# Performance work log

Hardware: AMD Instinct MI355X
Metric: run time of the kernel (lower is better)

Reference implementation:

```python
import jax, jax.numpy as jnp
import numpy as np

D_MODEL = 512
N_HEADS = 4
D_HEAD = D_MODEL // N_HEADS
D_FF = 2048
N_LAYERS = 3
IN_DIM = 25
OUT_DIM = 1
PRE = 20          # pre_training_size
SCALE = 10.0      # scaling_factor
EPS = 1e-5


def setup_inputs() -> dict:
    key = jax.random.key(0)
    ks = jax.random.split(key, 20)
    B, S = 4, 2048
    def gn(k, shape, fan_in):
        return jax.random.normal(k, shape, jnp.float32) * (1.0 / np.sqrt(fan_in))
    return {
        "src": jax.random.normal(ks[0], (B, S, IN_DIM), jnp.float32),
        "emb_w": gn(ks[1], (D_MODEL, IN_DIM), IN_DIM),
        "emb_b": jnp.zeros((D_MODEL,), jnp.float32),
        "in_w": gn(ks[2], (N_LAYERS, 3 * D_MODEL, D_MODEL), D_MODEL),
        "in_b": jnp.zeros((N_LAYERS, 3 * D_MODEL), jnp.float32),
        "out_w": gn(ks[3], (N_LAYERS, D_MODEL, D_MODEL), D_MODEL),
        "out_b": jnp.zeros((N_LAYERS, D_MODEL), jnp.float32),
        "ln1_g": jnp.ones((N_LAYERS, D_MODEL), jnp.float32),
        "ln1_b": jnp.zeros((N_LAYERS, D_MODEL), jnp.float32),
        "ln2_g": jnp.ones((N_LAYERS, D_MODEL), jnp.float32),
        "ln2_b": jnp.zeros((N_LAYERS, D_MODEL), jnp.float32),
        "ff1_w": gn(ks[4], (N_LAYERS, D_FF, D_MODEL), D_MODEL),
        "ff1_b": jnp.zeros((N_LAYERS, D_FF), jnp.float32),
        "ff2_w": gn(ks[5], (N_LAYERS, D_MODEL, D_FF), D_FF),
        "ff2_b": jnp.zeros((N_LAYERS, D_MODEL), jnp.float32),
        "dec_w": gn(ks[6], (OUT_DIM, D_MODEL), D_MODEL),
        "dec_b": jnp.zeros((OUT_DIM,), jnp.float32),
    }


def _layer_norm(x, g, b):
    mu = jnp.mean(x, axis=-1, keepdims=True)
    var = jnp.var(x, axis=-1, keepdims=True)
    return (x - mu) * jax.lax.rsqrt(var + EPS) * g + b


def _pos_encoding(seq_len):
    # eval mode: start index 0, no dropout
    pos = jnp.arange(seq_len, dtype=jnp.float32)[:, None]           # [S,1]
    div = jnp.exp(jnp.arange(0, D_MODEL, 2, dtype=jnp.float32) * (-np.log(10000.0) / D_MODEL))  # [D/2]
    ang = pos * div                                                  # [S,D/2]
    return jnp.stack([jnp.sin(ang), jnp.cos(ang)], axis=-1).reshape(seq_len, D_MODEL)


def _causal_mask(seq_len):
    row = jnp.arange(seq_len)[:, None]
    col = jnp.arange(seq_len)[None, :]
    mask = jnp.where(col <= row, 0.0, -jnp.inf).astype(jnp.float32)
    # include_training_period=True: first PRE x PRE block unmasked
    return mask.at[:PRE, :PRE].set(0.0)


def reference(src, emb_w, emb_b, in_w, in_b, out_w, out_b,
              ln1_g, ln1_b, ln2_g, ln2_b, ff1_w, ff1_b, ff2_w, ff2_b,
              dec_w, dec_b):
    B, S, _ = src.shape
    x = src @ emb_w.T + emb_b                    # [B,S,D]
    x = x + _pos_encoding(S)[None]
    mask = _causal_mask(S)                       # [S,S]
    scale = 1.0 / np.sqrt(D_HEAD)
    for l in range(N_LAYERS):
        # --- self-attention (post-norm, eager bmm+softmax+bmm path) ---
        qkv = x @ in_w[l].T + in_b[l]            # [B,S,3D]
        q, k, v = jnp.split(qkv, 3, axis=-1)
        q = q.reshape(B, S, N_HEADS, D_HEAD).transpose(0, 2, 1, 3)
        k = k.reshape(B, S, N_HEADS, D_HEAD).transpose(0, 2, 1, 3)
        v = v.reshape(B, S, N_HEADS, D_HEAD).transpose(0, 2, 1, 3)
        scores = jnp.einsum('bhqd,bhkd->bhqk', q, k) * scale + mask
        attn = jax.nn.softmax(scores, axis=-1)   # [B,H,S,S] (need_weights=True path)
        o = jnp.einsum('bhqk,bhkd->bhqd', attn, v)
        o = o.transpose(0, 2, 1, 3).reshape(B, S, D_MODEL)
        o = o @ out_w[l].T + out_b[l]
        x = _layer_norm(x + o, ln1_g[l], ln1_b[l])
        # --- FFN ---
        h = jax.nn.relu(x @ ff1_w[l].T + ff1_b[l])
        h = h @ ff2_w[l].T + ff2_b[l]
        x = _layer_norm(x + h, ln2_g[l], ln2_b[l])
    out = jnp.tanh(x @ dec_w.T + dec_b) * SCALE  # [B,S,1]
    return out
```

## Files before the change

kernel.cpp:

```cpp
#include <hip/hip_runtime.h>

#define S_LEN 2048
#define DMODEL 512

typedef __attribute__((ext_vector_type(8))) short bf16x8;
typedef __attribute__((ext_vector_type(4))) float f32x4;
typedef __attribute__((ext_vector_type(4))) unsigned short u16x4;
typedef __attribute__((ext_vector_type(8))) unsigned short u16x8;
typedef __attribute__((ext_vector_type(2))) unsigned int u32x2;

__device__ __forceinline__ unsigned short f2bf(float f) {
    unsigned int u = __float_as_uint(f);
    u += 0x7fff + ((u >> 16) & 1);
    return (unsigned short)(u >> 16);
}
__device__ __forceinline__ float bf2f(unsigned short h) {
    return __uint_as_float(((unsigned int)h) << 16);
}
__device__ __forceinline__ void gll16(const void* g, void* l) {
    __builtin_amdgcn_global_load_lds(
        (const __attribute__((address_space(1))) unsigned int*)g,
        (__attribute__((address_space(3))) unsigned int*)l, 16, 0, 0);
}

__global__ __launch_bounds__(256) void conv_bf16(const float4* __restrict__ in,
                                                 u16x4* __restrict__ out)
{
    int i = blockIdx.x * 256 + threadIdx.x;
    float4 v = in[i];
    u16x4 o = { f2bf(v.x), f2bf(v.y), f2bf(v.z), f2bf(v.w) };
    out[i] = o;
}

__global__ __launch_bounds__(256) void embed_kernel(
    const float* __restrict__ src, const float* __restrict__ ew,
    const float* __restrict__ eb, float* __restrict__ X,
    unsigned short* __restrict__ Xb)
{
    int rid = blockIdx.x;
    int s = rid & (S_LEN - 1);
    int tid = threadIdx.x;
    __shared__ float sr[25];
    if (tid < 25) sr[tid] = src[rid * 25 + tid];
    __syncthreads();
    #pragma unroll
    for (int rep = 0; rep < 2; rep++) {
        int d = tid + rep * 256;
        float a = eb[d];
        #pragma unroll
        for (int k = 0; k < 25; k++) a = fmaf(sr[k], ew[d * 25 + k], a);
        int i2 = d & ~1;
        float div = expf(-(float)i2 * (9.210340371976184f / 512.f));
        float ang = (float)s * div;
        a += (d & 1) ? cosf(ang) : sinf(ang);
        X[(size_t)rid * DMODEL + d] = a;
        Xb[(size_t)rid * DMODEL + d] = f2bf(a);
    }
}

template<int MODE, int BN>
__global__ __launch_bounds__(256) void gemm_bf16(
    const unsigned short* __restrict__ A, int lda,
    const unsigned short* __restrict__ W, int K,
    const float* __restrict__ bias,
    unsigned short* __restrict__ out, int ldc,
    unsigned short* __restrict__ out2)
{
    constexpr int NJ = BN / 32;
    __shared__ __align__(16) unsigned short As[128 * 64];
    __shared__ __align__(16) unsigned short Ws[BN * 64];
    int tid = threadIdx.x;
    int lane = tid & 63, w = tid >> 6;
    int g = lane >> 4, c15 = lane & 15;
    int wm = w >> 1, wn = w & 1;
    int bm, bn;
    if (BN == 64) {
        int raw = blockIdx.x;
        int lid = ((raw & 7) << 6) | (raw >> 3);
        bn = lid & 7; bm = lid >> 3;
    } else {
        bm = blockIdx.y; bn = blockIdx.x;
    }

    f32x4 acc[4][NJ];
    #pragma unroll
    for (int i = 0; i < 4; i++)
        #pragma unroll
        for (int j = 0; j < NJ; j++) acc[i][j] = (f32x4){0.f, 0.f, 0.f, 0.f};

    const int nk = K >> 6;
    for (int kk = 0; kk < nk; kk++) {
        __syncthreads();
        #pragma unroll
        for (int i = 0; i < 4; i++) {
            int chunk = tid + i * 256;
            int r = chunk >> 3, c = chunk & 7;
            int cs = c ^ (r & 7);
            gll16(A + (size_t)(bm * 128 + r) * lda + kk * 64 + cs * 8,
                  (void*)(As + chunk * 8));
        }
        #pragma unroll
        for (int i = 0; i < BN / 32; i++) {
            int chunk = tid + i * 256;
            int r = chunk >> 3, c = chunk & 7;
            int cs = c ^ (r & 7);
            gll16(W + (size_t)(bn * BN + r) * K + kk * 64 + cs * 8,
                  (void*)(Ws + chunk * 8));
        }
        __syncthreads();
        bf16x8 a[4][2], b[NJ][2];
        #pragma unroll
        for (int mi = 0; mi < 4; mi++) {
            int row = wm * 64 + mi * 16 + c15;
            #pragma unroll
            for (int h = 0; h < 2; h++) {
                int ck = (h * 4 + g) ^ (row & 7);
                a[mi][h] = *(const bf16x8*)((const char*)As + row * 128 + ck * 16);
            }
        }
        #pragma unroll
        for (int nj = 0; nj < NJ; nj++) {
            int row = wn * (BN / 2) + nj * 16 + c15;
            #pragma unroll
            for (int h = 0; h < 2; h++) {
                int ck = (h * 4 + g) ^ (row & 7);
                b[nj][h] = *(const bf16x8*)((const char*)Ws + row * 128 + ck * 16);
            }
        }
        __builtin_amdgcn_s_setprio(1);
        #pragma unroll
        for (int h = 0; h < 2; h++)
            #pragma unroll
            for (int mi = 0; mi < 4; mi++)
                #pragma unroll
                for (int nj = 0; nj < NJ; nj++)
                    acc[mi][nj] = __builtin_amdgcn_mfma_f32_16x16x32_bf16(
                        a[mi][h], b[nj][h], acc[mi][nj], 0, 0, 0);
        __builtin_amdgcn_s_setprio(0);
    }
    #pragma unroll
    for (int nj = 0; nj < NJ; nj++) {
        int colb = bn * BN + wn * (BN / 2) + nj * 16;
        float bv = bias[colb + c15];
        #pragma unroll
        for (int mi = 0; mi < 4; mi++) {
            int rowb = bm * 128 + wm * 64 + mi * 16 + g * 4;
            if (MODE == 3 && colb >= 1024) {
                int cv = colb - 1024 + c15;
                int hh = cv >> 7, d = cv & 127;
                int bb = rowb >> 11, t = rowb & (S_LEN - 1);
                u16x4 pk;
                #pragma unroll
                for (int r = 0; r < 4; r++) pk[r] = f2bf(acc[mi][nj][r] + bv);
                *(u16x4*)(out2 + ((size_t)(bb * 4 + hh) * 128 + d) * S_LEN + t) = pk;
            } else {
                #pragma unroll
                for (int r = 0; r < 4; r++) {
                    float v = acc[mi][nj][r] + bv;
                    if (MODE == 2) v = fmaxf(v, 0.f);
                    out[(size_t)(rowb + r) * ldc + colb + c15] = f2bf(v);
                }
            }
        }
    }
}

__global__ __launch_bounds__(256) void flash_attn(
    const unsigned short* __restrict__ QKb,
    const unsigned short* __restrict__ Vt,
    unsigned short* __restrict__ Ob,
    unsigned short* __restrict__ Opart,
    float* __restrict__ Mpart,
    float* __restrict__ Lpart)
{
    __shared__ __align__(16) unsigned short Ks[2][64 * 128];
    __shared__ __align__(16) unsigned short Vts[2][128 * 64];
    __shared__ __align__(16) unsigned short Plds[4][16 * 72];
    const float scale = 0.08838834764831845f;
    int tid = threadIdx.x;
    int lane = tid & 63, w = tid >> 6;
    int g = lane >> 4, c15 = lane & 15;
    int raw = blockIdx.x;
    int lid = (raw & 7) * 96 + (raw >> 3);
    int bh = lid / 48, idx = lid - bh * 48;
    int b = bh >> 2, h = bh & 3;
    int qb, kt0, nkt, split;
    if (idx < 16) { qb = idx; kt0 = 0; nkt = qb + 1; split = -1; }
    else {
        int s = idx - 16;
        qb = 16 + (s >> 1);
        int j = s & 1;
        int n = qb + 1, c0 = (n + 1) >> 1;
        kt0 = j ? c0 : 0;
        nkt = j ? (n - c0) : c0;
        split = bh * 32 + (qb - 16) * 2 + j;
    }

    bf16x8 q[4];
    {
        const unsigned short* qrow =
            QKb + (size_t)(b * S_LEN + qb * 64 + w * 16 + c15) * 1024 + h * 128;
        #pragma unroll
        for (int k0 = 0; k0 < 4; k0++) q[k0] = *(const bf16x8*)(qrow + k0 * 32 + g * 8);
    }
    f32x4 o[8];
    #pragma unroll
    for (int cd = 0; cd < 8; cd++) o[cd] = (f32x4){0.f, 0.f, 0.f, 0.f};
    float m = -3e38f, l = 0.f;

    auto stage = [&](int kt, int bi) {
        #pragma unroll
        for (int i = 0; i < 4; i++) {
            int chunk = tid + i * 256;
            int r = chunk >> 4, c = chunk & 15;
            int cs = (c & 8) | ((c ^ r) & 7);
            gll16(QKb + (size_t)(b * S_LEN + kt * 64 + r) * 1024 + 512 + h * 128 + cs * 8,
                  (void*)(Ks[bi] + chunk * 8));
        }
        #pragma unroll
        for (int i = 0; i < 4; i++) {
            int chunk = tid + i * 256;
            int r = chunk >> 3, c = chunk & 7;
            int cs = (c ^ r) & 7;
            gll16(Vt + ((size_t)(b * 4 + h) * 128 + r) * S_LEN + kt * 64 + cs * 8,
                  (void*)(Vts[bi] + chunk * 8));
        }
    };

    stage(kt0, 0);
    __syncthreads();
    int buf = 0;

    for (int t = 0; t < nkt; t++) {
        int kt = kt0 + t;
        if (t + 1 < nkt) stage(kt + 1, buf ^ 1);
        f32x4 sf[4];
        __builtin_amdgcn_s_setprio(1);
        #pragma unroll
        for (int c = 0; c < 4; c++) {
            sf[c] = (f32x4){0.f, 0.f, 0.f, 0.f};
            int tok16 = c * 16 + c15;
            #pragma unroll
            for (int k0 = 0; k0 < 4; k0++) {
                int ck = k0 * 4 + g;
                int cs = (ck & 8) | ((ck ^ tok16) & 7);
                bf16x8 kf = *(const bf16x8*)((const char*)Ks[buf] + tok16 * 256 + cs * 16);
                sf[c] = __builtin_amdgcn_mfma_f32_16x16x32_bf16(kf, q[k0], sf[c], 0, 0, 0);
            }
        }
        __builtin_amdgcn_s_setprio(0);
        if (kt == qb) {
            int qr = qb * 64 + w * 16 + c15;
            #pragma unroll
            for (int c = 0; c < 4; c++)
                #pragma unroll
                for (int r = 0; r < 4; r++) {
                    int tok = kt * 64 + c * 16 + g * 4 + r;
                    bool ok = (tok <= qr) || (qr < 20 && tok < 20);
                    if (!ok) sf[c][r] = -3e38f;
                }
        }
        float t0 = fmaxf(fmaxf(sf[0][0], sf[0][1]), fmaxf(sf[0][2], sf[0][3]));
        float t1 = fmaxf(fmaxf(sf[1][0], sf[1][1]), fmaxf(sf[1][2], sf[1][3]));
        float t2 = fmaxf(fmaxf(sf[2][0], sf[2][1]), fmaxf(sf[2][2], sf[2][3]));
        float t3 = fmaxf(fmaxf(sf[3][0], sf[3][1]), fmaxf(sf[3][2], sf[3][3]));
        float mt = fmaxf(fmaxf(t0, t1), fmaxf(t2, t3));
        mt = fmaxf(mt, __shfl_xor(mt, 16));
        mt = fmaxf(mt, __shfl_xor(mt, 32));
        bool need = !__all(mt <= m + 90.5f);
        float sc = 1.f;
        if (need) {
            float mn = fmaxf(m, mt);
            sc = __expf((m - mn) * scale);
            m = mn;
        }
        float msc = m * scale;
        #pragma unroll
        for (int c = 0; c < 4; c++)
            #pragma unroll
            for (int r = 0; r < 4; r++)
                sf[c][r] = __expf(fmaf(sf[c][r], scale, -msc));
        float s0 = (sf[0][0] + sf[0][1]) + (sf[0][2] + sf[0][3]);
        float s1 = (sf[1][0] + sf[1][1]) + (sf[1][2] + sf[1][3]);
        float s2 = (sf[2][0] + sf[2][1]) + (sf[2][2] + sf[2][3]);
        float s3 = (sf[3][0] + sf[3][1]) + (sf[3][2] + sf[3][3]);
        float ls = (s0 + s1) + (s2 + s3);
        ls += __shfl_xor(ls, 16);
        ls += __shfl_xor(ls, 32);
        if (need) l *= sc;
        l += ls;
        #pragma unroll
        for (int c = 0; c < 4; c++) {
            unsigned int lo = ((unsigned int)f2bf(sf[c][1]) << 16) | f2bf(sf[c][0]);
            unsigned int hi = ((unsigned int)f2bf(sf[c][3]) << 16) | f2bf(sf[c][2]);
            u32x2 pk = {lo, hi};
            *(u32x2*)&Plds[w][c15 * 72 + c * 16 + g * 4] = pk;
        }
        if (need) {
            float r0 = __shfl(sc, g * 4 + 0);
            float r1 = __shfl(sc, g * 4 + 1);
            float r2 = __shfl(sc, g * 4 + 2);
            float r3 = __shfl(sc, g * 4 + 3);
            #pragma unroll
            for (int cd = 0; cd < 8; cd++) {
                o[cd][0] *= r0; o[cd][1] *= r1; o[cd][2] *= r2; o[cd][3] *= r3;
            }
        }
        bf16x8 pa0 = *(const bf16x8*)((const char*)&Plds[w][0] + c15 * 144 + g * 16);
        bf16x8 pa1 = *(const bf16x8*)((const char*)&Plds[w][0] + c15 * 144 + 64 + g * 16);
        __builtin_amdgcn_s_setprio(1);
        #pragma unroll
        for (int cd = 0; cd < 8; cd++) {
            int dv = cd * 16 + c15;
            int csa = (g ^ dv) & 7;
            bf16x8 vfa = *(const bf16x8*)((const char*)Vts[buf] + dv * 128 + csa * 16);
            o[cd] = __builtin_amdgcn_mfma_f32_16x16x32_bf16(pa0, vfa, o[cd], 0, 0, 0);
            int csb = ((4 + g) ^ dv) & 7;
            bf16x8 vfb = *(const bf16x8*)((const char*)Vts[buf] + dv * 128 + csb * 16);
            o[cd] = __builtin_amdgcn_mfma_f32_16x16x32_bf16(pa1, vfb, o[cd], 0, 0, 0);
        }
        __builtin_amdgcn_s_setprio(0);
        __syncthreads();
        buf ^= 1;
    }

    if (split < 0) {
        float li0 = 1.f / __shfl(l, g * 4 + 0);
        float li1 = 1.f / __shfl(l, g * 4 + 1);
        float li2 = 1.f / __shfl(l, g * 4 + 2);
        float li3 = 1.f / __shfl(l, g * 4 + 3);
        size_t obase = (size_t)(b * S_LEN + qb * 64 + w * 16 + g * 4) * 512 + h * 128;
        #pragma unroll
        for (int cd = 0; cd < 8; cd++) {
            Ob[obase + 0 * 512 + cd * 16 + c15] = f2bf(o[cd][0] * li0);
            Ob[obase + 1 * 512 + cd * 16 + c15] = f2bf(o[cd][1] * li1);
            Ob[obase + 2 * 512 + cd * 16 + c15] = f2bf(o[cd][2] * li2);
            Ob[obase + 3 * 512 + cd * 16 + c15] = f2bf(o[cd][3] * li3);
        }
    } else {
        unsigned short* op = Opart + (size_t)split * 8192;
        int rb = w * 16 + g * 4;
        #pragma unroll
        for (int cd = 0; cd < 8; cd++) {
            op[(rb + 0) * 128 + cd * 16 + c15] = f2bf(o[cd][0]);
            op[(rb + 1) * 128 + cd * 16 + c15] = f2bf(o[cd][1]);
            op[(rb + 2) * 128 + cd * 16 + c15] = f2bf(o[cd][2]);
            op[(rb + 3) * 128 + cd * 16 + c15] = f2bf(o[cd][3]);
        }
        if (g == 0) {
            Mpart[split * 64 + w * 16 + c15] = m;
            Lpart[split * 64 + w * 16 + c15] = l;
        }
    }
}

__global__ __launch_bounds__(256) void attn_merge(
    const unsigned short* __restrict__ Opart,
    const float* __restrict__ Mpart, const float* __restrict__ Lpart,
    unsigned short* __restrict__ Ob)
{
    const float scale = 0.08838834764831845f;
    int bid = blockIdx.x;
    int bh = bid >> 4, qe = bid & 15;
    int qb = 16 + qe;
    int b = bh >> 2, h = bh & 3;
    int p0 = bh * 32 + qe * 2;
    int t = threadIdx.x;
    int r = t >> 2, dq = t & 3;
    float m0 = Mpart[p0 * 64 + r], m1 = Mpart[(p0 + 1) * 64 + r];
    float l0 = Lpart[p0 * 64 + r], l1 = Lpart[(p0 + 1) * 64 + r];
    float ms = fmaxf(m0, m1);
    float w0 = __expf((m0 - ms) * scale), w1 = __expf((m1 - ms) * scale);
    float linv = 1.f / (l0 * w0 + l1 * w1);
    w0 *= linv; w1 *= linv;
    const unsigned short* o0 = Opart + (size_t)p0 * 8192 + r * 128 + dq * 32;
    const unsigned short* o1 = o0 + 8192;
    unsigned short* od = Ob + (size_t)(b * S_LEN + qb * 64 + r) * 512 + h * 128 + dq * 32;
    #pragma unroll
    for (int i = 0; i < 4; i++) {
        u16x8 a = *(const u16x8*)(o0 + i * 8);
        u16x8 c = *(const u16x8*)(o1 + i * 8);
        u16x8 d;
        #pragma unroll
        for (int j = 0; j < 8; j++)
            d[j] = f2bf(bf2f(a[j]) * w0 + bf2f(c[j]) * w1);
        *(u16x8*)(od + i * 8) = d;
    }
}

__global__ __launch_bounds__(256) void add_ln_kernel(
    float* __restrict__ X, const unsigned short* __restrict__ D,
    const float* __restrict__ gw, const float* __restrict__ bw,
    unsigned short* __restrict__ Xb)
{
    int row = blockIdx.x;
    int tid = threadIdx.x;
    size_t base = (size_t)row * DMODEL;
    float v0 = X[base + tid] + bf2f(D[base + tid]);
    float v1 = X[base + tid + 256] + bf2f(D[base + tid + 256]);
    float s = v0 + v1;
    float sq = v0 * v0 + v1 * v1;
    #pragma unroll
    for (int off = 32; off > 0; off >>= 1) {
        s  += __shfl_down(s, off);
        sq += __shfl_down(sq, off);
    }
    __shared__ float red[2][4];
    int wv = tid >> 6;
    if ((tid & 63) == 0) { red[0][wv] = s; red[1][wv] = sq; }
    __syncthreads();
    s  = red[0][0] + red[0][1] + red[0][2] + red[0][3];
    sq = red[1][0] + red[1][1] + red[1][2] + red[1][3];
    float mu = s * (1.f / DMODEL);
    float var = sq * (1.f / DMODEL) - mu * mu;
    float rs = rsqrtf(var + 1e-5f);
    float y0 = (v0 - mu) * rs * gw[tid] + bw[tid];
    float y1 = (v1 - mu) * rs * gw[tid + 256] + bw[tid + 256];
    X[base + tid] = y0;
    X[base + tid + 256] = y1;
    Xb[base + tid] = f2bf(y0);
    Xb[base + tid + 256] = f2bf(y1);
}

__global__ __launch_bounds__(256) void decoder_kernel(
    const float* __restrict__ X, const float* __restrict__ w,
    const float* __restrict__ bias, float* __restrict__ out)
{
    int tid = threadIdx.x;
    int lane = tid & 63;
    int row = blockIdx.x * 4 + (tid >> 6);
    float s = 0.f;
    size_t base = (size_t)row * DMODEL;
    #pragma unroll
    for (int i = 0; i < 8; i++) s = fmaf(X[base + lane + i * 64], w[lane + i * 64], s);
    #pragma unroll
    for (int off = 32; off > 0; off >>= 1) s += __shfl_down(s, off);
    if (lane == 0) out[row] = tanhf(s + bias[0]) * 10.0f;
}

extern "C" void kernel_launch(void* const* d_in, const int* in_sizes, int n_in,
                              void* d_out, int out_size, void* d_ws, size_t ws_size,
                              hipStream_t stream)
{
    const float* src   = (const float*)d_in[0];
    const float* emb_w = (const float*)d_in[1];
    const float* emb_b = (const float*)d_in[2];
    const float* in_w  = (const float*)d_in[3];
    const float* in_b  = (const float*)d_in[4];
    const float* out_w = (const float*)d_in[5];
    const float* out_b = (const float*)d_in[6];
    const float* ln1_g = (const float*)d_in[7];
    const float* ln1_b = (const float*)d_in[8];
    const float* ln2_g = (const float*)d_in[9];
    const float* ln2_b = (const float*)d_in[10];
    const float* ff1_w = (const float*)d_in[11];
    const float* ff1_b = (const float*)d_in[12];
    const float* ff2_w = (const float*)d_in[13];
    const float* ff2_b = (const float*)d_in[14];
    const float* dec_w = (const float*)d_in[15];
    const float* dec_b = (const float*)d_in[16];

    char* ws = (char*)d_ws;
    float*          X   = (float*)ws;
    unsigned short* Xb  = (unsigned short*)(ws + (16u << 20));
    unsigned short* Pb  = (unsigned short*)(ws + (24u << 20));
    unsigned short* Ob  = (unsigned short*)(ws + (32u << 20));
    unsigned short* QKb = (unsigned short*)(ws + (40u << 20));
    unsigned short* Vt  = (unsigned short*)(ws + (56u << 20));
    unsigned short* Hb  = (unsigned short*)(ws + (40u << 20));
    unsigned short* Opart = (unsigned short*)(ws + (16u << 20));
    float* Mpart = (float*)(ws + (24u << 20));
    float* Lpart = Mpart + 512 * 64;
    unsigned short* in_wb  = (unsigned short*)(ws + (72u << 20));
    unsigned short* out_wb = in_wb  + 3u * 1536 * 512;
    unsigned short* ff1_wb = out_wb + 3u * 512 * 512;
    unsigned short* ff2_wb = ff1_wb + 3u * 2048 * 512;
    float* outp = (float*)d_out;
    const int M = 4 * S_LEN;

    conv_bf16<<<2304, 256, 0, stream>>>((const float4*)in_w,  (u16x4*)in_wb);
    conv_bf16<<<768,  256, 0, stream>>>((const float4*)out_w, (u16x4*)out_wb);
    conv_bf16<<<3072, 256, 0, stream>>>((const float4*)ff1_w, (u16x4*)ff1_wb);
    conv_bf16<<<3072, 256, 0, stream>>>((const float4*)ff2_w, (u16x4*)ff2_wb);

    embed_kernel<<<M, 256, 0, stream>>>(src, emb_w, emb_b, X, Xb);

    for (int l = 0; l < 3; l++) {
        gemm_bf16<3, 128><<<dim3(12, 64), 256, 0, stream>>>(
            Xb, 512, in_wb + (size_t)l * 1536 * 512, 512, in_b + l * 1536,
            QKb, 1024, Vt);
        flash_attn<<<768, 256, 0, stream>>>(QKb, Vt, Ob, Opart, Mpart, Lpart);
        attn_merge<<<256, 256, 0, stream>>>(Opart, Mpart, Lpart, Ob);
        gemm_bf16<1, 64><<<dim3(512), 256, 0, stream>>>(
            Ob, 512, out_wb + (size_t)l * 512 * 512, 512, out_b + l * 512,
            Pb, 512, nullptr);
        add_ln_kernel<<<M, 256, 0, stream>>>(X, Pb, ln1_g + l * 512, ln1_b + l * 512, Xb);
        gemm_bf16<2, 128><<<dim3(16, 64), 256, 0, stream>>>(
            Xb, 512, ff1_wb + (size_t)l * 2048 * 512, 512, ff1_b + l * 2048,
            Hb, 2048, nullptr);
        gemm_bf16<1, 64><<<dim3(512), 256, 0, stream>>>(
            Hb, 2048, ff2_wb + (size_t)l * 512 * 2048, 2048, ff2_b + l * 512,
            Pb, 512, nullptr);
        add_ln_kernel<<<M, 256, 0, stream>>>(X, Pb, ln2_g + l * 512, ln2_b + l * 512, Xb);
    }

    decoder_kernel<<<M / 4, 256, 0, stream>>>(X, dec_w, dec_b, outp);
}
```

Baseline: 571.5 us.

## Load K/V fragments directly from global in flash attention; merge weight conversions

Flash attention no longer stages K and V tiles into double-buffered LDS through global_load_lds. Each wave now reads its MFMA operand fragments straight from global memory (relying on cache) and drops the per-tile block barrier. This removes the LDS footprint and the synchronisation, which can raise occupancy. The cost is redundant global and cache traffic, since all four waves read the same K/V, plus exposed load latency with no prefetch. Separately, the four weight conversion launches are fused into one kernel to cut launch overhead.

```diff
diff --git a/kernel.cpp b/kernel.cpp
--- a/kernel.cpp
+++ b/kernel.cpp
@@ -23,13 +23,21 @@
         (__attribute__((address_space(3))) unsigned int*)l, 16, 0, 0);
 }
 
-__global__ __launch_bounds__(256) void conv_bf16(const float4* __restrict__ in,
-                                                 u16x4* __restrict__ out)
+__global__ __launch_bounds__(256) void conv_all(
+    const float4* __restrict__ in_w, const float4* __restrict__ out_w,
+    const float4* __restrict__ ff1_w, const float4* __restrict__ ff2_w,
+    u16x4* __restrict__ in_wb, u16x4* __restrict__ out_wb,
+    u16x4* __restrict__ ff1_wb, u16x4* __restrict__ ff2_wb)
 {
     int i = blockIdx.x * 256 + threadIdx.x;
-    float4 v = in[i];
+    const float4* src; u16x4* dst; int j;
+    if (i < 589824)        { src = in_w;  dst = in_wb;  j = i; }
+    else if (i < 786432)   { src = out_w; dst = out_wb; j = i - 589824; }
+    else if (i < 1572864)  { src = ff1_w; dst = ff1_wb; j = i - 786432; }
+    else                   { src = ff2_w; dst = ff2_wb; j = i - 1572864; }
+    float4 v = src[j];
     u16x4 o = { f2bf(v.x), f2bf(v.y), f2bf(v.z), f2bf(v.w) };
-    out[i] = o;
+    dst[j] = o;
 }
 
 __global__ __launch_bounds__(256) void embed_kernel(
@@ -173,8 +181,6 @@
     float* __restrict__ Mpart,
     float* __restrict__ Lpart)
 {
-    __shared__ __align__(16) unsigned short Ks[2][64 * 128];
-    __shared__ __align__(16) unsigned short Vts[2][128 * 64];
     __shared__ __align__(16) unsigned short Plds[4][16 * 72];
     const float scale = 0.08838834764831845f;
     int tid = threadIdx.x;
@@ -196,6 +202,9 @@
         split = bh * 32 + (qb - 16) * 2 + j;
     }
 
+    const unsigned short* Kbase = QKb + (size_t)b * S_LEN * 1024 + 512 + h * 128;
+    const unsigned short* Vbase = Vt + (size_t)(b * 4 + h) * 128 * S_LEN;
+
     bf16x8 q[4];
     {
         const unsigned short* qrow =
@@ -208,43 +217,17 @@
     for (int cd = 0; cd < 8; cd++) o[cd] = (f32x4){0.f, 0.f, 0.f, 0.f};
     float m = -3e38f, l = 0.f;
 
-    auto stage = [&](int kt, int bi) {
-        #pragma unroll
-        for (int i = 0; i < 4; i++) {
-            int chunk = tid + i * 256;
-            int r = chunk >> 4, c = chunk & 15;
-            int cs = (c & 8) | ((c ^ r) & 7);
-            gll16(QKb + (size_t)(b * S_LEN + kt * 64 + r) * 1024 + 512 + h * 128 + cs * 8,
-                  (void*)(Ks[bi] + chunk * 8));
-        }
-        #pragma unroll
-        for (int i = 0; i < 4; i++) {
-            int chunk = tid + i * 256;
-            int r = chunk >> 3, c = chunk & 7;
-            int cs = (c ^ r) & 7;
-            gll16(Vt + ((size_t)(b * 4 + h) * 128 + r) * S_LEN + kt * 64 + cs * 8,
-                  (void*)(Vts[bi] + chunk * 8));
-        }
-    };
-
-    stage(kt0, 0);
-    __syncthreads();
-    int buf = 0;
-
     for (int t = 0; t < nkt; t++) {
         int kt = kt0 + t;
-        if (t + 1 < nkt) stage(kt + 1, buf ^ 1);
         f32x4 sf[4];
         __builtin_amdgcn_s_setprio(1);
         #pragma unroll
         for (int c = 0; c < 4; c++) {
             sf[c] = (f32x4){0.f, 0.f, 0.f, 0.f};
-            int tok16 = c * 16 + c15;
+            const unsigned short* krow = Kbase + (size_t)(kt * 64 + c * 16 + c15) * 1024;
             #pragma unroll
             for (int k0 = 0; k0 < 4; k0++) {
-                int ck = k0 * 4 + g;
-                int cs = (ck & 8) | ((ck ^ tok16) & 7);
-                bf16x8 kf = *(const bf16x8*)((const char*)Ks[buf] + tok16 * 256 + cs * 16);
+                bf16x8 kf = *(const bf16x8*)(krow + (k0 * 4 + g) * 8);
                 sf[c] = __builtin_amdgcn_mfma_f32_16x16x32_bf16(kf, q[k0], sf[c], 0, 0, 0);
             }
         }
@@ -311,17 +294,13 @@
         __builtin_amdgcn_s_setprio(1);
         #pragma unroll
         for (int cd = 0; cd < 8; cd++) {
-            int dv = cd * 16 + c15;
-            int csa = (g ^ dv) & 7;
-            bf16x8 vfa = *(const bf16x8*)((const char*)Vts[buf] + dv * 128 + csa * 16);
+            const unsigned short* vrow = Vbase + (size_t)(cd * 16 + c15) * S_LEN + kt * 64;
+            bf16x8 vfa = *(const bf16x8*)(vrow + g * 8);
             o[cd] = __builtin_amdgcn_mfma_f32_16x16x32_bf16(pa0, vfa, o[cd], 0, 0, 0);
-            int csb = ((4 + g) ^ dv) & 7;
-            bf16x8 vfb = *(const bf16x8*)((const char*)Vts[buf] + dv * 128 + csb * 16);
+            bf16x8 vfb = *(const bf16x8*)(vrow + 32 + g * 8);
             o[cd] = __builtin_amdgcn_mfma_f32_16x16x32_bf16(pa1, vfb, o[cd], 0, 0, 0);
         }
         __builtin_amdgcn_s_setprio(0);
-        __syncthreads();
-        buf ^= 1;
     }
 
     if (split < 0) {
@@ -478,10 +457,10 @@
     float* outp = (float*)d_out;
     const int M = 4 * S_LEN;
 
-    conv_bf16<<<2304, 256, 0, stream>>>((const float4*)in_w,  (u16x4*)in_wb);
-    conv_bf16<<<768,  256, 0, stream>>>((const float4*)out_w, (u16x4*)out_wb);
-    conv_bf16<<<3072, 256, 0, stream>>>((const float4*)ff1_w, (u16x4*)ff1_wb);
-    conv_bf16<<<3072, 256, 0, stream>>>((const float4*)ff2_w, (u16x4*)ff2_wb);
+    conv_all<<<9216, 256, 0, stream>>>(
+        (const float4*)in_w, (const float4*)out_w,
+        (const float4*)ff1_w, (const float4*)ff2_w,
+        (u16x4*)in_wb, (u16x4*)out_wb, (u16x4*)ff1_wb, (u16x4*)ff2_wb);
 
     embed_kernel<<<M, 256, 0, stream>>>(src, emb_w, emb_b, X, Xb);
 
```

Result: slower. 881.2 us (+54.2%).
